# Kernel optimization log

Measured on AMD Instinct MI355X. Metric: run time of the kernel, lower is better.

The kernel has to match this reference:

```python
import jax, jax.numpy as jnp
import numpy as np

D_MODEL = 1024
NHEAD = 16
HEAD_DIM = D_MODEL // NHEAD
LN_EPS = 1e-5


def _retention_scan(v, lam_h):
    # v: (B, L, H, DH); lam_h: (H,)
    # recurrence: s_0 = v_0; s_t = lam * s_{t-1} + v_t
    B, L, H, DH = v.shape
    a = jnp.broadcast_to(lam_h[None, None, :, None], v.shape)

    def combine(x, y):
        a1, b1 = x
        a2, b2 = y
        return (a1 * a2, a2 * b1 + b2)

    _, states = jax.lax.associative_scan(combine, (a, v), axis=1)
    return states


def setup_inputs() -> dict:
    key = jax.random.key(0)
    ks = jax.random.split(key, 6)
    B, L, D = 4, 4096, D_MODEL
    s = 1.0 / np.sqrt(D)
    return {
        "x": jax.random.normal(ks[0], (B, L, D), jnp.float32),
        "Wq": jax.random.normal(ks[1], (D, D), jnp.float32) * s,
        "Wv": jax.random.normal(ks[2], (D, D), jnp.float32) * s,
        "Wg": jax.random.normal(ks[3], (D, D), jnp.float32) * s,
        "Wo": jax.random.normal(ks[4], (D, D), jnp.float32) * s,
        "beta": jnp.full((NHEAD,), -0.2, jnp.float32),
        "ln_gamma": jnp.ones((D_MODEL,), jnp.float32),
        "ln_beta": jnp.zeros((D_MODEL,), jnp.float32),
    }


def reference(x, Wq, Wv, Wg, Wo, beta, ln_gamma, ln_beta):
    B, L, D = x.shape
    H, DH = NHEAD, HEAD_DIM
    # projections (torch Linear: x @ W.T)
    q = (x @ Wq.T).reshape(B, L, H, DH)
    v = (x @ Wv.T).reshape(B, L, H, DH)
    lam_h = jax.nn.sigmoid(beta)
    state = _retention_scan(v, lam_h)  # (B, L, H, DH)
    y = (q * state).reshape(B, L, D)
    # LayerNorm over last dim
    mu = jnp.mean(y, axis=-1, keepdims=True)
    var = jnp.mean((y - mu) ** 2, axis=-1, keepdims=True)
    y = (y - mu) * jax.lax.rsqrt(var + LN_EPS) * ln_gamma + ln_beta
    # SiLU gate
    gate = jax.nn.silu(x @ Wg.T)
    y = y * gate
    return y @ Wo.T
```

## Files before the change

### kernel.cpp

```cpp
#include <hip/hip_runtime.h>

#define BB 4
#define LL 4096
#define DM 1024
#define NH 16
#define MM (BB * LL)
#define CC2 256
#define LC2 16

typedef unsigned short u16;
typedef float f32x4 __attribute__((ext_vector_type(4)));
typedef __bf16 mfma_in __attribute__((ext_vector_type(8)));

__device__ __forceinline__ u16 f2bf(float f) {
    unsigned u = __float_as_uint(f);
    u += 0x7FFFu + ((u >> 16) & 1u);
    return (u16)(u >> 16);
}
__device__ __forceinline__ float bf2f(u16 u) {
    return __uint_as_float(((unsigned)u) << 16);
}

__device__ __forceinline__ void gld_lds16(const u16* g, u16* l) {
    __builtin_amdgcn_global_load_lds(
        (const __attribute__((address_space(1))) void*)g,
        (__attribute__((address_space(3))) void*)l,
        16, 0, 0);
}

#define XF4 (MM * DM / 4)
#define WF4 (DM * DM / 4)
__global__ __launch_bounds__(256)
void cvt_all(const float* __restrict__ x,
             const float* __restrict__ w0, const float* __restrict__ w1,
             const float* __restrict__ w2, const float* __restrict__ w3,
             u16* __restrict__ dst) {
    int i = blockIdx.x * 256 + threadIdx.x;
    const float* src;
    int si;
    if (i < XF4) { src = x; si = i; }
    else {
        int j = i - XF4;
        const float* ws[4] = {w0, w1, w2, w3};
        src = ws[j >> 18];
        si = j & (WF4 - 1);
    }
    float4 f = ((const float4*)src)[si];
    ushort4 o;
    o.x = f2bf(f.x); o.y = f2bf(f.y); o.z = f2bf(f.z); o.w = f2bf(f.w);
    ((ushort4*)dst)[i] = o;
}

__device__ __forceinline__ void mainloop_bk64(
    const u16* __restrict__ A, const u16* __restrict__ B, int K,
    int mBlk, int nBlk, u16* As, u16* Bs, f32x4 acc[4][4]) {
    const int tid  = threadIdx.x;
    const int wave = tid >> 6;
    const int lane = tid & 63;
    const int quad = lane >> 4;
    const int l16  = lane & 15;
    const int wm   = (wave >> 1) * 64;
    const int wn   = (wave & 1) * 64;

    const int srow8 = wave * 8 + (lane >> 3);
    const int cOff  = ((lane & 7) ^ (lane >> 3)) * 8;

    const u16* gA[4];
    const u16* gB[4];
    u16* lA[4];
    u16* lB[4];
#pragma unroll
    for (int j = 0; j < 4; j++) {
        gA[j] = A + (size_t)(mBlk + j * 32 + srow8) * K + cOff;
        gB[j] = B + (size_t)(nBlk + j * 32 + srow8) * K + cOff;
        lA[j] = As + (j * 32 + wave * 8) * 64;
        lB[j] = Bs + (j * 32 + wave * 8) * 64;
    }

    int rowA[4], rowB[4];
#pragma unroll
    for (int i = 0; i < 4; i++) {
        rowA[i] = (wm + i * 16 + l16) * 64;
        rowB[i] = (wn + i * 16 + l16) * 64;
    }
    const int c0 = ((quad    ) ^ (l16 & 7)) * 8;
    const int c1 = ((quad + 4) ^ (l16 & 7)) * 8;

    for (int kt = 0; kt < K; kt += 64) {
        __syncthreads();
#pragma unroll
        for (int j = 0; j < 4; j++) gld_lds16(gA[j] + kt, lA[j]);
#pragma unroll
        for (int j = 0; j < 4; j++) gld_lds16(gB[j] + kt, lB[j]);
        __syncthreads();

#pragma unroll
        for (int s = 0; s < 2; s++) {
            const int cs = s ? c1 : c0;
            mfma_in af[4], bfr[4];
#pragma unroll
            for (int i = 0; i < 4; i++)
                af[i] = *(const mfma_in*)&As[rowA[i] + cs];
#pragma unroll
            for (int j = 0; j < 4; j++)
                bfr[j] = *(const mfma_in*)&Bs[rowB[j] + cs];
#pragma unroll
            for (int i = 0; i < 4; i++)
#pragma unroll
                for (int j = 0; j < 4; j++)
                    acc[i][j] = __builtin_amdgcn_mfma_f32_16x16x32_bf16(af[i], bfr[j], acc[i][j], 0, 0, 0);
        }
    }
}

__global__ __launch_bounds__(256)
void gemm_qvg(const u16* __restrict__ A, const u16* __restrict__ B,
              u16* __restrict__ oq, u16* __restrict__ ov, u16* __restrict__ og,
              int K) {
    __shared__ u16 As[128 * 64];
    __shared__ u16 Bs[128 * 64];
    const int mBlk = blockIdx.x * 128;
    const int nBlk = blockIdx.y * 128;

    f32x4 acc[4][4] = {};
    mainloop_bk64(A, B, K, mBlk, nBlk, As, Bs, acc);

    const int tid  = threadIdx.x;
    const int wave = tid >> 6;
    const int lane = tid & 63;
    const int quad = lane >> 4;
    const int l16  = lane & 15;
    const int wm   = (wave >> 1) * 64;
    const int wn   = (wave & 1) * 64;

    u16* outs[3] = {oq, ov, og};
    u16* O = outs[nBlk >> 10];
    const int nIn = nBlk & 1023;
#pragma unroll
    for (int i = 0; i < 4; i++) {
        int row0 = mBlk + wm + i * 16 + quad * 4;
#pragma unroll
        for (int j = 0; j < 4; j++) {
            int col = nIn + wn + j * 16 + l16;
#pragma unroll
            for (int r = 0; r < 4; r++)
                O[(size_t)(row0 + r) * DM + col] = f2bf(acc[i][j][r]);
        }
    }
}

__global__ __launch_bounds__(256)
void gemm_out(const u16* __restrict__ A, const u16* __restrict__ B,
              float* __restrict__ C, int N, int K) {
    __shared__ u16 As[128 * 64];
    __shared__ u16 Bs[128 * 64];
    const int mBlk = blockIdx.x * 128;
    const int nBlk = blockIdx.y * 128;

    f32x4 acc[4][4] = {};
    mainloop_bk64(A, B, K, mBlk, nBlk, As, Bs, acc);

    const int tid  = threadIdx.x;
    const int wave = tid >> 6;
    const int lane = tid & 63;
    const int quad = lane >> 4;
    const int l16  = lane & 15;
    const int wm   = (wave >> 1) * 64;
    const int wn   = (wave & 1) * 64;

#pragma unroll
    for (int i = 0; i < 4; i++) {
        int row0 = mBlk + wm + i * 16 + quad * 4;
#pragma unroll
        for (int j = 0; j < 4; j++) {
            int col = nBlk + wn + j * 16 + l16;
#pragma unroll
            for (int r = 0; r < 4; r++)
                C[(size_t)(row0 + r) * N + col] = acc[i][j][r];
        }
    }
}

__global__ __launch_bounds__(256)
void scan_ends(const u16* __restrict__ v, const float* __restrict__ beta,
               float* __restrict__ ebuf) {
    int d = blockIdx.x * 256 + threadIdx.x;
    int c = blockIdx.y, b = blockIdx.z;
    int h = d >> 6;
    float lam = 1.0f / (1.0f + __expf(-beta[h]));
    size_t idx = ((size_t)b * LL + (size_t)c * LC2) * DM + d;
    float s = 0.0f;
#pragma unroll
    for (int i = 0; i < LC2; i++) {
        s = lam * s + bf2f(v[idx]);
        idx += DM;
    }
    ebuf[((size_t)b * CC2 + c) * DM + d] = s;
}

__global__ __launch_bounds__(256)
void scan_carry(const float* __restrict__ ebuf, const float* __restrict__ beta,
                float* __restrict__ carry) {
    int ch = blockIdx.x * 256 + threadIdx.x;
    int b = ch >> 10, d = ch & 1023;
    int h = d >> 6;
    float lam = 1.0f / (1.0f + __expf(-beta[h]));
    float lamC = lam;
    for (int i = 0; i < 4; i++) lamC *= lamC;
    float cur = 0.0f;
#pragma unroll 8
    for (int c = 0; c < CC2; c++) {
        size_t idx = ((size_t)b * CC2 + c) * DM + d;
        carry[idx] = cur;
        cur = lamC * cur + ebuf[idx];
    }
}

__global__ __launch_bounds__(256)
void scan_ln_gate(const u16* __restrict__ v, const u16* __restrict__ q,
                  const u16* __restrict__ g, const float* __restrict__ carry,
                  const float* __restrict__ beta, const float* __restrict__ gamma,
                  const float* __restrict__ lnb, u16* __restrict__ out) {
    __shared__ float red[2][8];
    const int t = threadIdx.x;
    const int c = blockIdx.x, b = blockIdx.y;
    const int wave = t >> 6, lane = t & 63;
    const int d0 = t * 4;
    const int h = d0 >> 6;
    float lam = 1.0f / (1.0f + __expf(-beta[h]));
    float4 gm = ((const float4*)gamma)[t];
    float4 bt = ((const float4*)lnb)[t];
    float4 cr = *(const float4*)(carry + ((size_t)b * CC2 + c) * DM + d0);
    float s0 = cr.x, s1 = cr.y, s2 = cr.z, s3 = cr.w;
    size_t base = ((size_t)b * LL + (size_t)c * LC2) * DM + d0;

    for (int i = 0; i < LC2; i++) {
        ushort4 v4 = *(const ushort4*)(v + base);
        ushort4 q4 = *(const ushort4*)(q + base);
        ushort4 g4 = *(const ushort4*)(g + base);
        s0 = lam * s0 + bf2f(v4.x);
        s1 = lam * s1 + bf2f(v4.y);
        s2 = lam * s2 + bf2f(v4.z);
        s3 = lam * s3 + bf2f(v4.w);
        float y0 = bf2f(q4.x) * s0, y1 = bf2f(q4.y) * s1;
        float y2 = bf2f(q4.z) * s2, y3 = bf2f(q4.w) * s3;
        float sum = y0 + y1 + y2 + y3;
        float sq  = y0 * y0 + y1 * y1 + y2 * y2 + y3 * y3;
#pragma unroll
        for (int off = 32; off > 0; off >>= 1) {
            sum += __shfl_xor(sum, off);
            sq  += __shfl_xor(sq, off);
        }
        int p = i & 1;
        if (lane == 0) { red[p][wave] = sum; red[p][4 + wave] = sq; }
        __syncthreads();
        float ts = red[p][0] + red[p][1] + red[p][2] + red[p][3];
        float tq = red[p][4] + red[p][5] + red[p][6] + red[p][7];
        float mu  = ts * (1.0f / DM);
        float inv = rsqrtf(tq * (1.0f / DM) - mu * mu + 1e-5f);

        float gv0 = bf2f(g4.x), gv1 = bf2f(g4.y), gv2 = bf2f(g4.z), gv3 = bf2f(g4.w);
        float x0 = ((y0 - mu) * inv * gm.x + bt.x) * (gv0 / (1.0f + __expf(-gv0)));
        float x1 = ((y1 - mu) * inv * gm.y + bt.y) * (gv1 / (1.0f + __expf(-gv1)));
        float x2 = ((y2 - mu) * inv * gm.z + bt.z) * (gv2 / (1.0f + __expf(-gv2)));
        float x3 = ((y3 - mu) * inv * gm.w + bt.w) * (gv3 / (1.0f + __expf(-gv3)));
        ushort4 o;
        o.x = f2bf(x0); o.y = f2bf(x1); o.z = f2bf(x2); o.w = f2bf(x3);
        *(ushort4*)(out + base) = o;
        base += DM;
    }
}

extern "C" void kernel_launch(void* const* d_in, const int* in_sizes, int n_in,
                              void* d_out, int out_size, void* d_ws, size_t ws_size,
                              hipStream_t stream) {
    const float* x     = (const float*)d_in[0];
    const float* Wq    = (const float*)d_in[1];
    const float* Wv    = (const float*)d_in[2];
    const float* Wg    = (const float*)d_in[3];
    const float* Wo    = (const float*)d_in[4];
    const float* beta  = (const float*)d_in[5];
    const float* gamma = (const float*)d_in[6];
    const float* lnb   = (const float*)d_in[7];

    u16* xb  = (u16*)d_ws;
    u16* Wqb = xb + (size_t)MM * DM;
    u16* Wob = Wqb + (size_t)3 * DM * DM;
    u16* qb  = Wob + (size_t)DM * DM;
    u16* vb  = qb + (size_t)MM * DM;
    u16* gb  = vb + (size_t)MM * DM;
    float* ebuf  = (float*)(gb + (size_t)MM * DM);
    float* carry = ebuf + (size_t)BB * CC2 * DM;
    u16* yfin = xb;

    cvt_all<<<(XF4 + 4 * WF4 + 255) / 256, 256, 0, stream>>>(x, Wq, Wv, Wg, Wo, xb);

    dim3 gq(MM / 128, 3 * DM / 128);
    gemm_qvg<<<gq, 256, 0, stream>>>(xb, Wqb, qb, vb, gb, DM);

    dim3 gs(DM / 256, CC2, BB);
    scan_ends<<<gs, 256, 0, stream>>>(vb, beta, ebuf);
    scan_carry<<<(BB * DM) / 256, 256, 0, stream>>>(ebuf, beta, carry);
    dim3 gf(CC2, BB);
    scan_ln_gate<<<gf, 256, 0, stream>>>(vb, qb, gb, carry, beta, gamma, lnb, yfin);

    dim3 go(MM / 128, DM / 128);
    gemm_out<<<go, 256, 0, stream>>>(yfin, Wob, (float*)d_out, DM, DM);
}
```

Baseline: 352.2 us.

## Use 256x256 double-buffered ping-pong GEMM mainloop with 8 waves

Both projection GEMMs move from 128x128 tiles with 4 waves and a single LDS buffer to 256x256 tiles with 8 waves. The new mainloop double-buffers A and B in LDS and interleaves global-to-LDS prefetch of the next K slice with MFMA quadrants, using barriers, explicit waitcnt and s_setprio. The aim is to hide memory latency behind compute and raise arithmetic intensity per loaded byte. In exchange it uses 128KB of LDS per block, which limits occupancy to one block per CU. The final iteration also issues harmless wrapped prefetch loads.

```diff
diff --git a/kernel.cpp b/kernel.cpp
--- a/kernel.cpp
+++ b/kernel.cpp
@@ -7,6 +7,9 @@
 #define MM (BB * LL)
 #define CC2 256
 #define LC2 16
+
+#define BKT 64
+#define NKT (DM / BKT)
 
 typedef unsigned short u16;
 typedef float f32x4 __attribute__((ext_vector_type(4)));
@@ -51,93 +54,178 @@
     ((ushort4*)dst)[i] = o;
 }
 
-__device__ __forceinline__ void mainloop_bk64(
-    const u16* __restrict__ A, const u16* __restrict__ B, int K,
-    int mBlk, int nBlk, u16* As, u16* Bs, f32x4 acc[4][4]) {
+
+template<int IOFF, int JOFF>
+__device__ __forceinline__ void mfmaQ(const mfma_in (&a)[4][2], const mfma_in (&b)[2][2],
+                                      f32x4 (&acc)[8][4]) {
+#pragma unroll
+    for (int s = 0; s < 2; s++)
+#pragma unroll
+        for (int i = 0; i < 4; i++)
+#pragma unroll
+            for (int j = 0; j < 2; j++)
+                acc[IOFF + i][JOFF + j] = __builtin_amdgcn_mfma_f32_16x16x32_bf16(
+                    a[i][s], b[j][s], acc[IOFF + i][JOFF + j], 0, 0, 0);
+}
+
+#define PH_MID() do { \
+    __builtin_amdgcn_s_barrier(); \
+    asm volatile("s_waitcnt lgkmcnt(0)" ::: "memory"); \
+    __builtin_amdgcn_sched_barrier(0); \
+    __builtin_amdgcn_s_setprio(1); \
+} while (0)
+
+#define PH_END() do { \
+    __builtin_amdgcn_s_setprio(0); \
+    __builtin_amdgcn_sched_barrier(0); \
+    __builtin_amdgcn_s_barrier(); \
+} while (0)
+
+#define PH_END_VM() do { \
+    __builtin_amdgcn_s_setprio(0); \
+    __builtin_amdgcn_sched_barrier(0); \
+    asm volatile("s_waitcnt vmcnt(4)" ::: "memory"); \
+    __builtin_amdgcn_s_barrier(); \
+} while (0)
+
+__device__ __forceinline__ void mainloop256(
+    const u16* __restrict__ A, const u16* __restrict__ B,
+    int mBlk, int nBlk,
+    u16 (*__restrict__ As)[256 * 64], u16 (*__restrict__ Bs)[256 * 64],
+    f32x4 (&acc)[8][4]) {
     const int tid  = threadIdx.x;
     const int wave = tid >> 6;
     const int lane = tid & 63;
     const int quad = lane >> 4;
     const int l16  = lane & 15;
-    const int wm   = (wave >> 1) * 64;
-    const int wn   = (wave & 1) * 64;
-
-    const int srow8 = wave * 8 + (lane >> 3);
-    const int cOff  = ((lane & 7) ^ (lane >> 3)) * 8;
-
-    const u16* gA[4];
-    const u16* gB[4];
-    u16* lA[4];
-    u16* lB[4];
-#pragma unroll
-    for (int j = 0; j < 4; j++) {
-        gA[j] = A + (size_t)(mBlk + j * 32 + srow8) * K + cOff;
-        gB[j] = B + (size_t)(nBlk + j * 32 + srow8) * K + cOff;
-        lA[j] = As + (j * 32 + wave * 8) * 64;
-        lB[j] = Bs + (j * 32 + wave * 8) * 64;
-    }
-
-    int rowA[4], rowB[4];
-#pragma unroll
-    for (int i = 0; i < 4; i++) {
-        rowA[i] = (wm + i * 16 + l16) * 64;
-        rowB[i] = (wn + i * 16 + l16) * 64;
-    }
+    const int wm   = (wave >> 2) * 128;
+    const int wn   = (wave & 3) * 64;
+
+    const int sRow = wave * 8 + (lane >> 3);
+    const int sCol = ((lane & 7) ^ (lane >> 3)) * 8;
+    const u16* gA = A + (size_t)(mBlk + sRow) * DM + sCol;
+    const u16* gB = B + (size_t)(nBlk + sRow) * DM + sCol;
+    const int ldsW = wave * 8 * 64;
+
+    int rA[8], rB[4];
+#pragma unroll
+    for (int i = 0; i < 8; i++) rA[i] = (wm + i * 16 + l16) * 64;
+#pragma unroll
+    for (int j = 0; j < 4; j++) rB[j] = (wn + j * 16 + l16) * 64;
     const int c0 = ((quad    ) ^ (l16 & 7)) * 8;
     const int c1 = ((quad + 4) ^ (l16 & 7)) * 8;
 
-    for (int kt = 0; kt < K; kt += 64) {
-        __syncthreads();
-#pragma unroll
-        for (int j = 0; j < 4; j++) gld_lds16(gA[j] + kt, lA[j]);
-#pragma unroll
-        for (int j = 0; j < 4; j++) gld_lds16(gB[j] + kt, lB[j]);
-        __syncthreads();
-
-#pragma unroll
-        for (int s = 0; s < 2; s++) {
-            const int cs = s ? c1 : c0;
-            mfma_in af[4], bfr[4];
-#pragma unroll
-            for (int i = 0; i < 4; i++)
-                af[i] = *(const mfma_in*)&As[rowA[i] + cs];
-#pragma unroll
-            for (int j = 0; j < 4; j++)
-                bfr[j] = *(const mfma_in*)&Bs[rowB[j] + cs];
-#pragma unroll
-            for (int i = 0; i < 4; i++)
-#pragma unroll
-                for (int j = 0; j < 4; j++)
-                    acc[i][j] = __builtin_amdgcn_mfma_f32_16x16x32_bf16(af[i], bfr[j], acc[i][j], 0, 0, 0);
-        }
-    }
-}
-
-__global__ __launch_bounds__(256)
+#define STG_A(buf, h, t) do { \
+    const int kk_ = ((t) & (NKT - 1)) * BKT; \
+    gld_lds16(gA + (size_t)((h) * 128) * DM + kk_,      &As[buf][((h) * 128) * 64 + ldsW]); \
+    gld_lds16(gA + (size_t)((h) * 128 + 64) * DM + kk_, &As[buf][((h) * 128 + 64) * 64 + ldsW]); \
+} while (0)
+#define STG_B(buf, h, t) do { \
+    const int kk_ = ((t) & (NKT - 1)) * BKT; \
+    gld_lds16(gB + (size_t)((h) * 128) * DM + kk_,      &Bs[buf][((h) * 128) * 64 + ldsW]); \
+    gld_lds16(gB + (size_t)((h) * 128 + 64) * DM + kk_, &Bs[buf][((h) * 128 + 64) * 64 + ldsW]); \
+} while (0)
+#define LDA(dst, buf, i, s) (dst) = *(const mfma_in*)&As[buf][rA[i] + ((s) ? c1 : c0)]
+#define LDB(dst, buf, j, s) (dst) = *(const mfma_in*)&Bs[buf][rB[j] + ((s) ? c1 : c0)]
+
+    mfma_in aL[4][2], aH[4][2], bL[2][2], bH[2][2];
+
+    STG_A(0, 0, 0); STG_A(0, 1, 0);
+    STG_B(0, 0, 0); STG_B(0, 1, 0);
+    STG_A(1, 0, 1); STG_A(1, 1, 1);
+    asm volatile("s_waitcnt vmcnt(4)" ::: "memory");
+    __builtin_amdgcn_s_barrier();
+
+#pragma unroll 1
+    for (int it = 0; it < NKT / 2; ++it) {
+        const int k = 2 * it;
+
+#pragma unroll
+        for (int i = 0; i < 4; i++) { LDA(aL[i][0], 0, i, 0); LDA(aL[i][1], 0, i, 1); }
+#pragma unroll
+        for (int j = 0; j < 2; j++) { LDB(bL[j][0], 0, j, 0); LDB(bL[j][1], 0, j, 1); }
+        STG_B(1, 0, k + 1);
+        PH_MID();
+        mfmaQ<0, 0>(aL, bL, acc);
+        PH_END();
+
+#pragma unroll
+        for (int i = 0; i < 4; i++) { LDA(aH[i][0], 0, i + 4, 0); LDA(aH[i][1], 0, i + 4, 1); }
+        STG_B(1, 1, k + 1);
+        PH_MID();
+        mfmaQ<4, 0>(aH, bL, acc);
+        PH_END();
+
+#pragma unroll
+        for (int j = 0; j < 2; j++) { LDB(bH[j][0], 0, j + 2, 0); LDB(bH[j][1], 0, j + 2, 1); }
+        STG_A(0, 0, k + 2);
+        PH_MID();
+        mfmaQ<0, 2>(aL, bH, acc);
+        PH_END();
+
+        STG_A(0, 1, k + 2);
+        PH_MID();
+        mfmaQ<4, 2>(aH, bH, acc);
+        PH_END_VM();
+
+#pragma unroll
+        for (int i = 0; i < 4; i++) { LDA(aL[i][0], 1, i, 0); LDA(aL[i][1], 1, i, 1); }
+#pragma unroll
+        for (int j = 0; j < 2; j++) { LDB(bL[j][0], 1, j, 0); LDB(bL[j][1], 1, j, 1); }
+        STG_B(0, 0, k + 2);
+        PH_MID();
+        mfmaQ<0, 0>(aL, bL, acc);
+        PH_END();
+
+#pragma unroll
+        for (int i = 0; i < 4; i++) { LDA(aH[i][0], 1, i + 4, 0); LDA(aH[i][1], 1, i + 4, 1); }
+        STG_B(0, 1, k + 2);
+        PH_MID();
+        mfmaQ<4, 0>(aH, bL, acc);
+        PH_END();
+
+#pragma unroll
+        for (int j = 0; j < 2; j++) { LDB(bH[j][0], 1, j + 2, 0); LDB(bH[j][1], 1, j + 2, 1); }
+        STG_A(1, 0, k + 3);
+        PH_MID();
+        mfmaQ<0, 2>(aL, bH, acc);
+        PH_END();
+
+        STG_A(1, 1, k + 3);
+        PH_MID();
+        mfmaQ<4, 2>(aH, bH, acc);
+        PH_END_VM();
+    }
+#undef STG_A
+#undef STG_B
+#undef LDA
+#undef LDB
+}
+
+__global__ __launch_bounds__(512, 2)
 void gemm_qvg(const u16* __restrict__ A, const u16* __restrict__ B,
-              u16* __restrict__ oq, u16* __restrict__ ov, u16* __restrict__ og,
-              int K) {
-    __shared__ u16 As[128 * 64];
-    __shared__ u16 Bs[128 * 64];
-    const int mBlk = blockIdx.x * 128;
-    const int nBlk = blockIdx.y * 128;
-
-    f32x4 acc[4][4] = {};
-    mainloop_bk64(A, B, K, mBlk, nBlk, As, Bs, acc);
+              u16* __restrict__ oq, u16* __restrict__ ov, u16* __restrict__ og) {
+    __shared__ __align__(16) u16 As[2][256 * 64];
+    __shared__ __align__(16) u16 Bs[2][256 * 64];
+    const int mBlk = blockIdx.x * 256;
+    const int nBlk = blockIdx.y * 256;
+
+    f32x4 acc[8][4] = {};
+    mainloop256(A, B, mBlk, nBlk, As, Bs, acc);
 
     const int tid  = threadIdx.x;
     const int wave = tid >> 6;
     const int lane = tid & 63;
     const int quad = lane >> 4;
     const int l16  = lane & 15;
-    const int wm   = (wave >> 1) * 64;
-    const int wn   = (wave & 1) * 64;
+    const int wm   = (wave >> 2) * 128;
+    const int wn   = (wave & 3) * 64;
 
     u16* outs[3] = {oq, ov, og};
     u16* O = outs[nBlk >> 10];
     const int nIn = nBlk & 1023;
 #pragma unroll
-    for (int i = 0; i < 4; i++) {
+    for (int i = 0; i < 8; i++) {
         int row0 = mBlk + wm + i * 16 + quad * 4;
 #pragma unroll
         for (int j = 0; j < 4; j++) {
@@ -149,34 +237,34 @@
     }
 }
 
-__global__ __launch_bounds__(256)
+__global__ __launch_bounds__(512, 2)
 void gemm_out(const u16* __restrict__ A, const u16* __restrict__ B,
-              float* __restrict__ C, int N, int K) {
-    __shared__ u16 As[128 * 64];
-    __shared__ u16 Bs[128 * 64];
-    const int mBlk = blockIdx.x * 128;
-    const int nBlk = blockIdx.y * 128;
-
-    f32x4 acc[4][4] = {};
-    mainloop_bk64(A, B, K, mBlk, nBlk, As, Bs, acc);
+              float* __restrict__ C) {
+    __shared__ __align__(16) u16 As[2][256 * 64];
+    __shared__ __align__(16) u16 Bs[2][256 * 64];
+    const int mBlk = blockIdx.x * 256;
+    const int nBlk = blockIdx.y * 256;
+
+    f32x4 acc[8][4] = {};
+    mainloop256(A, B, mBlk, nBlk, As, Bs, acc);
 
     const int tid  = threadIdx.x;
     const int wave = tid >> 6;
     const int lane = tid & 63;
     const int quad = lane >> 4;
     const int l16  = lane & 15;
-    const int wm   = (wave >> 1) * 64;
-    const int wn   = (wave & 1) * 64;
-
-#pragma unroll
-    for (int i = 0; i < 4; i++) {
+    const int wm   = (wave >> 2) * 128;
+    const int wn   = (wave & 3) * 64;
+
+#pragma unroll
+    for (int i = 0; i < 8; i++) {
         int row0 = mBlk + wm + i * 16 + quad * 4;
 #pragma unroll
         for (int j = 0; j < 4; j++) {
             int col = nBlk + wn + j * 16 + l16;
 #pragma unroll
             for (int r = 0; r < 4; r++)
-                C[(size_t)(row0 + r) * N + col] = acc[i][j][r];
+                C[(size_t)(row0 + r) * DM + col] = acc[i][j][r];
         }
     }
 }
@@ -295,8 +383,8 @@
 
     cvt_all<<<(XF4 + 4 * WF4 + 255) / 256, 256, 0, stream>>>(x, Wq, Wv, Wg, Wo, xb);
 
-    dim3 gq(MM / 128, 3 * DM / 128);
-    gemm_qvg<<<gq, 256, 0, stream>>>(xb, Wqb, qb, vb, gb, DM);
+    dim3 gq(MM / 256, 3 * DM / 256);
+    gemm_qvg<<<gq, 512, 0, stream>>>(xb, Wqb, qb, vb, gb);
 
     dim3 gs(DM / 256, CC2, BB);
     scan_ends<<<gs, 256, 0, stream>>>(vb, beta, ebuf);
@@ -304,6 +392,6 @@
     dim3 gf(CC2, BB);
     scan_ln_gate<<<gf, 256, 0, stream>>>(vb, qb, gb, carry, beta, gamma, lnb, yfin);
 
-    dim3 go(MM / 128, DM / 128);
-    gemm_out<<<go, 256, 0, stream>>>(yfin, Wob, (float*)d_out, DM, DM);
-}
+    dim3 go(MM / 256, DM / 256);
+    gemm_out<<<go, 512, 0, stream>>>(yfin, Wob, (float*)d_out);
+}
```

Measured after the change: 337.8 us. -4.1%, faster.
